# Kernel tuning notes

Measured on AMD Instinct MI355X. Metric: run time of the kernel, lower is better.

Reference implementation:

```python
import jax, jax.numpy as jnp
import numpy as np

N_NODES = 100000
N_EDGES = 1600000
N_GRAPHS = 2048
EPS = 1e-5


def gcn_conv(x, src, dst, W, b):
    # PyG GCNConv: add self-loops, symmetric normalization D^-1/2 (A+I) D^-1/2, then linear.
    xw = x @ W  # [N, F]
    deg = jax.ops.segment_sum(jnp.ones((src.shape[0],), xw.dtype), dst, num_segments=N_NODES) + 1.0
    dinv = jax.lax.rsqrt(deg)  # deg >= 1 due to self loops
    norm = dinv[src] * dinv[dst]  # [E]
    msg = xw[src] * norm[:, None]  # gather + scale
    agg = jax.ops.segment_sum(msg, dst, num_segments=N_NODES)
    agg = agg + xw * (dinv * dinv)[:, None]  # self-loop term
    return agg + b


def bn_eval(h, gamma, beta, rm, rv):
    return (h - rm) * jax.lax.rsqrt(rv + EPS) * gamma + beta


def setup_inputs() -> dict:
    key = jax.random.key(0)
    ks = jax.random.split(key, 12)
    x = jax.random.normal(ks[0], (N_NODES, 74), jnp.float32)
    edge_index = jax.random.randint(ks[1], (2, N_EDGES), 0, N_NODES, dtype=jnp.int64)
    batch = jnp.sort(jax.random.randint(ks[2], (N_NODES,), 0, N_GRAPHS, dtype=jnp.int64))
    def lin(k, fi, fo):
        return jax.random.normal(k, (fi, fo), jnp.float32) / np.sqrt(fi)
    return {
        "x": x, "edge_index": edge_index, "batch": batch,
        "W1": lin(ks[3], 74, 256), "b1": jnp.zeros((256,), jnp.float32),
        "g1": jnp.ones((256,), jnp.float32), "beta1": jnp.zeros((256,), jnp.float32),
        "rm1": jax.random.normal(ks[4], (256,), jnp.float32) * 0.1,
        "rv1": jax.random.uniform(ks[5], (256,), jnp.float32, 0.5, 1.5),
        "W2": lin(ks[6], 256, 256), "b2": jnp.zeros((256,), jnp.float32),
        "g2": jnp.ones((256,), jnp.float32), "beta2": jnp.zeros((256,), jnp.float32),
        "rm2": jax.random.normal(ks[7], (256,), jnp.float32) * 0.1,
        "rv2": jax.random.uniform(ks[8], (256,), jnp.float32, 0.5, 1.5),
        "W3": lin(ks[9], 256, 384), "b3": jnp.zeros((384,), jnp.float32),
    }


def reference(x, edge_index, batch, W1, b1, g1, beta1, rm1, rv1,
              W2, b2, g2, beta2, rm2, rv2, W3, b3):
    src, dst = edge_index[0], edge_index[1]
    h1 = jax.nn.relu(bn_eval(gcn_conv(x, src, dst, W1, b1), g1, beta1, rm1, rv1))
    h2 = jax.nn.relu(bn_eval(gcn_conv(h1, src, dst, W2, b2), g2, beta2, rm2, rv2))
    h3 = gcn_conv(h2, src, dst, W3, b3)
    # global_mean_pool + global_max_pool over batch segments
    cnt = jax.ops.segment_sum(jnp.ones((N_NODES,), h3.dtype), batch, num_segments=N_GRAPHS)
    mean_pool = jax.ops.segment_sum(h3, batch, num_segments=N_GRAPHS) / jnp.maximum(cnt, 1.0)[:, None]
    max_pool = jax.ops.segment_max(h3, batch, num_segments=N_GRAPHS)
    return mean_pool + max_pool
```

## Files before the change

### kernel.cpp

```cpp
#include <hip/hip_runtime.h>

typedef __bf16 bf16x8 __attribute__((ext_vector_type(8)));
typedef float f32x4 __attribute__((ext_vector_type(4)));
typedef float f32x2 __attribute__((ext_vector_type(2)));
typedef unsigned short ushort4v __attribute__((ext_vector_type(4)));
typedef unsigned short ushort8v __attribute__((ext_vector_type(8)));

__device__ __forceinline__ unsigned short f2b(float f) {
  unsigned u = __float_as_uint(f);
  unsigned r = u + 0x7FFFu + ((u >> 16) & 1u);
  return (unsigned short)(r >> 16);
}
__device__ __forceinline__ float b2f(unsigned short v) {
  return __uint_as_float(((unsigned)v) << 16);
}

__device__ __forceinline__ void fp8x4_to_f32(unsigned w, float out[4]) {
#if __has_builtin(__builtin_amdgcn_cvt_pk_f32_fp8)
  f32x2 lo = __builtin_amdgcn_cvt_pk_f32_fp8(w, false);
  f32x2 hi = __builtin_amdgcn_cvt_pk_f32_fp8(w, true);
  out[0] = lo[0]; out[1] = lo[1]; out[2] = hi[0]; out[3] = hi[1];
#else
#pragma unroll
  for (int i = 0; i < 4; ++i) {
    unsigned u = (w >> (8 * i)) & 0xffu;
    unsigned em = u & 0x7fu;
    float nrm = __uint_as_float((em + 960u) << 20);
    float sub = (float)em * 0x1p-9f;
    float mag = (em >= 8u) ? nrm : sub;
    out[i] = (u & 0x80u) ? -mag : mag;
  }
#endif
}

__device__ __forceinline__ unsigned char f32_to_fp8(float f) {
  float a = fabsf(f);
  unsigned s = (__float_as_uint(f) >> 31) << 7;
  a = fminf(a, 448.0f);
  unsigned r;
  if (a >= 0x1p-6f) {
    unsigned b = __float_as_uint(a);
    unsigned m = b & 0x7fffffu;
    int ei = (int)(b >> 23) - 127;
    unsigned mr = (m + 0x80000u) >> 20;
    unsigned ee = (unsigned)(ei + 7) + (mr >> 3);
    mr &= 7u;
    if (ee >= 16u) { ee = 15u; mr = 6u; }
    r = (ee << 3) | mr;
  } else {
    unsigned m = (unsigned)(a * 512.0f + 0.5f);
    r = m;
  }
  return (unsigned char)(s | r);
}

static constexpr int SCAN_CHUNK = 1024;

__global__ void k_bnprep(const float* __restrict__ g, const float* __restrict__ beta,
                         const float* __restrict__ rm, const float* __restrict__ rv,
                         const float* __restrict__ b, int n,
                         float* __restrict__ scale, float* __restrict__ shift) {
  int i = blockIdx.x * blockDim.x + threadIdx.x;
  if (i < n) {
    float s = g[i] * rsqrtf(rv[i] + 1e-5f);
    scale[i] = s;
    shift[i] = (b[i] - rm[i]) * s + beta[i];
  }
}

__global__ void k_edge_count(const int* __restrict__ dst, int E, int* __restrict__ cnt) {
  int i = blockIdx.x * blockDim.x + threadIdx.x;
  if (i < E) atomicAdd(&cnt[dst[i]], 1);
}

__global__ void k_dinv(const int* __restrict__ cnt, int n, float* __restrict__ dinv) {
  int i = blockIdx.x * blockDim.x + threadIdx.x;
  if (i < n) dinv[i] = rsqrtf(1.0f + (float)cnt[i]);
}

__global__ void k_wt(const float* __restrict__ W, int K, int N, int Kp,
                     unsigned short* __restrict__ Wt) {
  int idx = blockIdx.x * blockDim.x + threadIdx.x;
  if (idx >= N * Kp) return;
  int n = idx / Kp, k = idx - n * Kp;
  Wt[idx] = f2b(k < K ? W[(size_t)k * N + n] : 0.0f);
}

__global__ void k_x2b(const float* __restrict__ x, const float* __restrict__ dinv, int n,
                      unsigned short* __restrict__ xb) {
  int idx = blockIdx.x * blockDim.x + threadIdx.x;
  if (idx >= n * 20) return;
  int row = idx / 20, j = idx - row * 20;
  int f0 = j * 4;
  float dv = dinv[row];
  ushort4v o;
#pragma unroll
  for (int j2 = 0; j2 < 4; ++j2) {
    int f = f0 + j2;
    o[j2] = (f < 74) ? f2b(dv * x[(size_t)row * 74 + f]) : (unsigned short)0;
  }
  *(ushort4v*)(xb + (size_t)row * 80 + f0) = o;
}

__global__ void k_gbounds(const int* __restrict__ batch, int n, int* __restrict__ gstart,
                          int* __restrict__ gend) {
  int i = blockIdx.x * blockDim.x + threadIdx.x;
  if (i >= n) return;
  int g = batch[i];
  if (i == 0 || batch[i - 1] != g) gstart[g] = i;
  if (i == n - 1 || batch[i + 1] != g) gend[g] = i + 1;
}

__global__ void k_chunk_sum(const int* __restrict__ cnt, int n, int* __restrict__ bsum) {
  __shared__ int s[256];
  int base = blockIdx.x * SCAN_CHUNK;
  int t = threadIdx.x;
  int v = 0;
  for (int i = t; i < SCAN_CHUNK; i += 256) {
    int idx = base + i;
    v += (idx < n) ? cnt[idx] : 0;
  }
  s[t] = v;
  __syncthreads();
  for (int o = 128; o > 0; o >>= 1) {
    if (t < o) s[t] += s[t + o];
    __syncthreads();
  }
  if (t == 0) bsum[blockIdx.x] = s[0];
}

__global__ void k_scan_bsum(int* __restrict__ bsum, int nb) {
  if (threadIdx.x == 0 && blockIdx.x == 0) {
    int acc = 0;
    for (int i = 0; i < nb; ++i) { int v = bsum[i]; bsum[i] = acc; acc += v; }
  }
}

__global__ void k_write_rowptr(const int* __restrict__ cnt, int n, const int* __restrict__ bsum,
                               int* __restrict__ rowptr, int E) {
  __shared__ int s[256];
  __shared__ int sx[257];
  int base = blockIdx.x * SCAN_CHUNK;
  int t = threadIdx.x;
  int loc[4];
  int sum = 0;
#pragma unroll
  for (int j = 0; j < 4; ++j) {
    int idx = base + t * 4 + j;
    int c = (idx < n) ? cnt[idx] : 0;
    loc[j] = sum;
    sum += c;
  }
  s[t] = sum;
  __syncthreads();
  if (t == 0) {
    int acc = 0;
    for (int i = 0; i < 256; ++i) { sx[i] = acc; acc += s[i]; }
  }
  __syncthreads();
  int off = bsum[blockIdx.x] + sx[t];
#pragma unroll
  for (int j = 0; j < 4; ++j) {
    int idx = base + t * 4 + j;
    if (idx < n) rowptr[idx] = off + loc[j];
  }
  if (blockIdx.x == 0 && t == 0) rowptr[n] = E;
}

__global__ void k_fill(const int* __restrict__ src, const int* __restrict__ dst, int E,
                       const int* __restrict__ rowptr, int* __restrict__ cursor,
                       int* __restrict__ colA) {
  int e = blockIdx.x * blockDim.x + threadIdx.x;
  if (e < E) {
    int d = dst[e];
    int p = atomicAdd(&cursor[d], 1);
    colA[rowptr[d] + p] = src[e];
  }
}

__global__ __launch_bounds__(256) void k_aggregate74b(const unsigned short* __restrict__ xb,
                                                      const int* __restrict__ rowptr,
                                                      const int* __restrict__ colA,
                                                      const float* __restrict__ dinv, int n,
                                                      unsigned short* __restrict__ out) {
  int wid = (int)((blockIdx.x * (size_t)blockDim.x + threadIdx.x) >> 6);
  int lane = threadIdx.x & 63;
  if (wid >= n) return;
  int half = lane >> 5, hl = lane & 31;
  bool act = hl < 20;
  float acc[4] = {0.0f, 0.0f, 0.0f, 0.0f};
  int e0 = rowptr[wid], e1 = rowptr[wid + 1];
  int e = e0;
  for (; e + 7 < e1; e += 8) {
    int b = e + half * 4;
    int s0 = colA[b], s1 = colA[b + 1], s2 = colA[b + 2], s3 = colA[b + 3];
    ushort4v v0 = {}, v1 = {}, v2 = {}, v3 = {};
    if (act) {
      v0 = *(const ushort4v*)(xb + (size_t)s0 * 80 + hl * 4);
      v1 = *(const ushort4v*)(xb + (size_t)s1 * 80 + hl * 4);
      v2 = *(const ushort4v*)(xb + (size_t)s2 * 80 + hl * 4);
      v3 = *(const ushort4v*)(xb + (size_t)s3 * 80 + hl * 4);
    }
#pragma unroll
    for (int j = 0; j < 4; ++j)
      acc[j] += (b2f(v0[j]) + b2f(v1[j])) + (b2f(v2[j]) + b2f(v3[j]));
  }
  for (int t = e + half; t < e1; t += 2) {
    int s = colA[t];
    ushort4v v = {};
    if (act) v = *(const ushort4v*)(xb + (size_t)s * 80 + hl * 4);
#pragma unroll
    for (int j = 0; j < 4; ++j) acc[j] += b2f(v[j]);
  }
#pragma unroll
  for (int j = 0; j < 4; ++j) acc[j] += __shfl_xor(acc[j], 32);
  if (half == 0) {
    float di = dinv[wid];
    if (act) {
      ushort4v sv = *(const ushort4v*)(xb + (size_t)wid * 80 + hl * 4);
      ushort4v o;
#pragma unroll
      for (int j = 0; j < 4; ++j) o[j] = f2b(di * (acc[j] + b2f(sv[j])));
      *(ushort4v*)(out + (size_t)wid * 128 + hl * 4) = o;
    } else {
      ushort4v z = {};
      *(ushort4v*)(out + (size_t)wid * 128 + 80 + (hl - 20) * 4) = z;
    }
  }
}

__global__ __launch_bounds__(256) void k_aggregate256(const unsigned char* __restrict__ h8,
                                                      const int* __restrict__ rowptr,
                                                      const int* __restrict__ colA,
                                                      const float* __restrict__ dinv, int n,
                                                      unsigned short* __restrict__ out) {
  int wid = (int)((blockIdx.x * (size_t)blockDim.x + threadIdx.x) >> 6);
  int lane = threadIdx.x & 63;
  if (wid >= n) return;
  float acc[4];
  {
    unsigned w = *(const unsigned*)(h8 + (size_t)wid * 256 + lane * 4);
    fp8x4_to_f32(w, acc);
  }
  int e0 = rowptr[wid], e1 = rowptr[wid + 1];
  int e = e0;
  for (; e + 7 < e1; e += 8) {
    int c[8];
    unsigned w[8];
#pragma unroll
    for (int q = 0; q < 8; ++q) c[q] = colA[e + q];
#pragma unroll
    for (int q = 0; q < 8; ++q)
      w[q] = *(const unsigned*)(h8 + (size_t)c[q] * 256 + lane * 4);
#pragma unroll
    for (int q = 0; q < 8; ++q) {
      float v[4];
      fp8x4_to_f32(w[q], v);
#pragma unroll
      for (int j = 0; j < 4; ++j) acc[j] += v[j];
    }
  }
  for (; e < e1; ++e) {
    unsigned w = *(const unsigned*)(h8 + (size_t)colA[e] * 256 + lane * 4);
    float v[4];
    fp8x4_to_f32(w, v);
#pragma unroll
    for (int j = 0; j < 4; ++j) acc[j] += v[j];
  }
  float di = dinv[wid];
  ushort4v o;
#pragma unroll
  for (int j = 0; j < 4; ++j) o[j] = f2b(di * acc[j]);
  *(ushort4v*)(out + (size_t)wid * 256 + lane * 4) = o;
}

template <int EPI>
__global__ __launch_bounds__(256) void k_gemm_mfma(const unsigned short* __restrict__ A,
                                                   const unsigned short* __restrict__ Bt,
                                                   int M, int N, int K,
                                                   const float* __restrict__ scale,
                                                   const float* __restrict__ shift,
                                                   const float* __restrict__ dinv,
                                                   unsigned char* __restrict__ C8,
                                                   unsigned short* __restrict__ C16) {
  __shared__ __align__(16) unsigned short Ast[128 * 64];
  __shared__ __align__(16) unsigned short Bst[64 * 64];
  const int t = threadIdx.x;
  const int lane = t & 63;
  const int wid = t >> 6;
  const int wm = wid >> 1, wn = wid & 1;
  const int lr = lane >> 4, lc = lane & 15;
  const int m0 = blockIdx.y * 128;
  const int n0 = blockIdx.x * 64;
  f32x4 acc[4][2] = {};
  char* astB = (char*)Ast;
  char* bstB = (char*)Bst;

  for (int kb = 0; kb < K; kb += 64) {
#pragma unroll
    for (int i = 0; i < 4; ++i) {
      int c = t + 256 * i;
      int row = c >> 3, slot = c & 7;
      int gm = m0 + row;
      ushort8v v = {};
      if (gm < M) v = *(const ushort8v*)(A + (size_t)gm * K + kb + slot * 8);
      int byte = row * 128 + slot * 16;
      *(ushort8v*)(astB + (byte ^ ((row & 7) << 4))) = v;
    }
#pragma unroll
    for (int i = 0; i < 2; ++i) {
      int c = t + 256 * i;
      int row = c >> 3, slot = c & 7;
      ushort8v v = *(const ushort8v*)(Bt + (size_t)(n0 + row) * K + kb + slot * 8);
      int byte = row * 128 + slot * 16;
      *(ushort8v*)(bstB + (byte ^ ((row & 7) << 4))) = v;
    }
    __syncthreads();
#pragma unroll
    for (int kk = 0; kk < 2; ++kk) {
      bf16x8 a[4], b[2];
      int kbyte = lr * 16 + kk * 64;
#pragma unroll
      for (int mi = 0; mi < 4; ++mi) {
        int row = wm * 64 + mi * 16 + lc;
        int byte = row * 128 + kbyte;
        a[mi] = *(const bf16x8*)(astB + (byte ^ ((row & 7) << 4)));
      }
#pragma unroll
      for (int ni = 0; ni < 2; ++ni) {
        int row = wn * 32 + ni * 16 + lc;
        int byte = row * 128 + kbyte;
        b[ni] = *(const bf16x8*)(bstB + (byte ^ ((row & 7) << 4)));
      }
#pragma unroll
      for (int mi = 0; mi < 4; ++mi)
#pragma unroll
        for (int ni = 0; ni < 2; ++ni)
          acc[mi][ni] =
              __builtin_amdgcn_mfma_f32_16x16x32_bf16(a[mi], b[ni], acc[mi][ni], 0, 0, 0);
    }
    __syncthreads();
  }

#pragma unroll
  for (int ni = 0; ni < 2; ++ni) {
    int colx = n0 + wn * 32 + ni * 16 + lc;
    float sc = (EPI == 0) ? scale[colx] : 0.0f;
    float sh = shift[colx];
#pragma unroll
    for (int mi = 0; mi < 4; ++mi) {
      int rbase = m0 + wm * 64 + mi * 16 + lr * 4;
#pragma unroll
      for (int r = 0; r < 4; ++r) {
        int row = rbase + r;
        if (row < M) {
          float v = acc[mi][ni][r];
          if (EPI == 0) {
            v = fmaxf(fmaf(v, sc, sh), 0.0f) * dinv[row];
            C8[(size_t)row * N + colx] = f32_to_fp8(v);
          } else {
            v += sh;
            C16[(size_t)row * N + colx] = f2b(v);
          }
        }
      }
    }
  }
}

__global__ __launch_bounds__(384) void k_pool(const unsigned short* __restrict__ h3,
                                              const int* __restrict__ gstart,
                                              const int* __restrict__ gend, int NF,
                                              float* __restrict__ out) {
  int g = blockIdx.x;
  int t = threadIdx.x;
  int s = gstart[g], e = gend[g];
  if (s >= 0 && e > s) {
    float sum = 0.0f, mx = -3.4e38f;
    for (int r = s; r < e; ++r) {
      float v = b2f(h3[(size_t)r * NF + t]);
      sum += v;
      mx = fmaxf(mx, v);
    }
    out[(size_t)g * NF + t] = sum / (float)(e - s) + mx;
  } else {
    out[(size_t)g * NF + t] = -INFINITY;
  }
}

extern "C" void kernel_launch(void* const* d_in, const int* in_sizes, int n_in, void* d_out,
                              int out_size, void* d_ws, size_t ws_size, hipStream_t stream) {
  const float* x    = (const float*)d_in[0];
  const int* edge   = (const int*)d_in[1];
  const int* batch  = (const int*)d_in[2];
  const float* W1   = (const float*)d_in[3];
  const float* b1   = (const float*)d_in[4];
  const float* g1   = (const float*)d_in[5];
  const float* be1  = (const float*)d_in[6];
  const float* rm1  = (const float*)d_in[7];
  const float* rv1  = (const float*)d_in[8];
  const float* W2   = (const float*)d_in[9];
  const float* b2   = (const float*)d_in[10];
  const float* g2   = (const float*)d_in[11];
  const float* be2  = (const float*)d_in[12];
  const float* rm2  = (const float*)d_in[13];
  const float* rv2  = (const float*)d_in[14];
  const float* W3   = (const float*)d_in[15];
  const float* b3   = (const float*)d_in[16];

  const int NN = in_sizes[2];
  const int E  = in_sizes[1] / 2;
  const int F1 = in_sizes[4];
  const int F3 = in_sizes[16];
  const int NG = out_size / F3;
  const int K1p = 128;
  const int* srcv = edge;
  const int* dstv = edge + E;

  char* p = (char*)d_ws;
  auto carve = [&](size_t bytes) -> char* {
    char* r = p;
    p += (bytes + 255) & ~(size_t)255;
    return r;
  };
  float* dinv           = (float*)carve((size_t)NN * 4);
  int* cnt              = (int*)carve((size_t)NN * 4);
  int* rowptr           = (int*)carve((size_t)(NN + 1) * 4);
  int* cursor           = (int*)carve((size_t)NN * 4);
  int* bsum             = (int*)carve(4096);
  int* colA             = (int*)carve((size_t)E * 4);
  float* scale1         = (float*)carve((size_t)F1 * 4);
  float* shift1         = (float*)carve((size_t)F1 * 4);
  float* scale2         = (float*)carve((size_t)F1 * 4);
  float* shift2         = (float*)carve((size_t)F1 * 4);
  unsigned short* W1t   = (unsigned short*)carve((size_t)F1 * K1p * 2);
  unsigned short* W2t   = (unsigned short*)carve((size_t)F1 * F1 * 2);
  unsigned short* W3t   = (unsigned short*)carve((size_t)F3 * F1 * 2);
  int* gstart           = (int*)carve((size_t)NG * 4);
  int* gend             = (int*)carve((size_t)NG * 4);
  unsigned short* xb    = (unsigned short*)carve((size_t)NN * 80 * 2);
  unsigned char* h8     = (unsigned char*)carve((size_t)NN * F1);
  unsigned short* agg   = (unsigned short*)carve((size_t)NN * F1 * 2);
  unsigned short* h3    = (unsigned short*)carve((size_t)NN * F3 * 2);
  (void)ws_size; (void)n_in;

  hipMemsetAsync(cnt, 0, (size_t)NN * 4, stream);
  hipMemsetAsync(cursor, 0, (size_t)NN * 4, stream);
  hipMemsetAsync(gstart, 0xFF, (size_t)NG * 4, stream);
  hipMemsetAsync(gend, 0, (size_t)NG * 4, stream);
  k_bnprep<<<1, 256, 0, stream>>>(g1, be1, rm1, rv1, b1, F1, scale1, shift1);
  k_bnprep<<<1, 256, 0, stream>>>(g2, be2, rm2, rv2, b2, F1, scale2, shift2);
  k_wt<<<(F1 * K1p + 255) / 256, 256, 0, stream>>>(W1, 74, F1, K1p, W1t);
  k_wt<<<(F1 * F1 + 255) / 256, 256, 0, stream>>>(W2, F1, F1, F1, W2t);
  k_wt<<<(F3 * F1 + 255) / 256, 256, 0, stream>>>(W3, F1, F3, F1, W3t);
  k_gbounds<<<(NN + 255) / 256, 256, 0, stream>>>(batch, NN, gstart, gend);

  k_edge_count<<<(E + 255) / 256, 256, 0, stream>>>(dstv, E, cnt);
  k_dinv<<<(NN + 255) / 256, 256, 0, stream>>>(cnt, NN, dinv);
  k_x2b<<<(NN * 20 + 255) / 256, 256, 0, stream>>>(x, dinv, NN, xb);

  int nchunks = (NN + SCAN_CHUNK - 1) / SCAN_CHUNK;
  k_chunk_sum<<<nchunks, 256, 0, stream>>>(cnt, NN, bsum);
  k_scan_bsum<<<1, 64, 0, stream>>>(bsum, nchunks);
  k_write_rowptr<<<nchunks, 256, 0, stream>>>(cnt, NN, bsum, rowptr, E);
  k_fill<<<(E + 255) / 256, 256, 0, stream>>>(srcv, dstv, E, rowptr, cursor, colA);

  dim3 blk(256);
  int aggBlocks = (NN + 3) / 4;
  int gy = (NN + 127) / 128;

  k_aggregate74b<<<aggBlocks, blk, 0, stream>>>(xb, rowptr, colA, dinv, NN, agg);
  {
    dim3 grid(F1 / 64, gy);
    k_gemm_mfma<0><<<grid, blk, 0, stream>>>(agg, W1t, NN, F1, K1p, scale1, shift1, dinv,
                                             h8, nullptr);
  }
  k_aggregate256<<<aggBlocks, blk, 0, stream>>>(h8, rowptr, colA, dinv, NN, agg);
  {
    dim3 grid(F1 / 64, gy);
    k_gemm_mfma<0><<<grid, blk, 0, stream>>>(agg, W2t, NN, F1, F1, scale2, shift2, dinv,
                                             h8, nullptr);
  }
  k_aggregate256<<<aggBlocks, blk, 0, stream>>>(h8, rowptr, colA, dinv, NN, agg);
  {
    dim3 grid(F3 / 64, gy);
    k_gemm_mfma<1><<<grid, blk, 0, stream>>>(agg, W3t, NN, F3, F1, nullptr, b3, dinv,
                                             nullptr, h3);
  }
  k_pool<<<NG, 384, 0, stream>>>(h3, gstart, gend, F3, (float*)d_out);
}
```

Before: 744.5 us.

## Build CSR via two-level bucketing by destination with shared-memory local scan

Replaces the global count/scan/fill CSR construction with a bucket pass that packs (src, local dst) per 128-node bucket, a single-block scan of bucket sizes, and a per-bucket kernel that counts, scans and scatters edges in shared memory while also computing dinv. This cuts global atomics on per-node counters and several kernel launches. It risks silently dropping edges if a bucket exceeds its fixed capacity. It also caps the scan at 1024 buckets and source ids at 17 bits, and reuses the h3 buffer as scratch.

```diff
diff --git a/kernel.cpp b/kernel.cpp
--- a/kernel.cpp
+++ b/kernel.cpp
@@ -54,7 +54,8 @@
   return (unsigned char)(s | r);
 }
 
-static constexpr int SCAN_CHUNK = 1024;
+static constexpr int BUCKET_NODES = 128;
+static constexpr int BUCKET_CAP = 4096;
 
 __global__ void k_bnprep(const float* __restrict__ g, const float* __restrict__ beta,
                          const float* __restrict__ rm, const float* __restrict__ rv,
@@ -68,16 +69,6 @@
   }
 }
 
-__global__ void k_edge_count(const int* __restrict__ dst, int E, int* __restrict__ cnt) {
-  int i = blockIdx.x * blockDim.x + threadIdx.x;
-  if (i < E) atomicAdd(&cnt[dst[i]], 1);
-}
-
-__global__ void k_dinv(const int* __restrict__ cnt, int n, float* __restrict__ dinv) {
-  int i = blockIdx.x * blockDim.x + threadIdx.x;
-  if (i < n) dinv[i] = rsqrtf(1.0f + (float)cnt[i]);
-}
-
 __global__ void k_wt(const float* __restrict__ W, int K, int N, int Kp,
                      unsigned short* __restrict__ Wt) {
   int idx = blockIdx.x * blockDim.x + threadIdx.x;
@@ -111,70 +102,79 @@
   if (i == n - 1 || batch[i + 1] != g) gend[g] = i + 1;
 }
 
-__global__ void k_chunk_sum(const int* __restrict__ cnt, int n, int* __restrict__ bsum) {
-  __shared__ int s[256];
-  int base = blockIdx.x * SCAN_CHUNK;
+__global__ void k_bucket(const int* __restrict__ src, const int* __restrict__ dst, int E,
+                         int* __restrict__ bcur, unsigned* __restrict__ bdata) {
+  int i = blockIdx.x * blockDim.x + threadIdx.x;
+  if (i < E) {
+    int d = dst[i];
+    int b = d >> 7;
+    int dl = d & 127;
+    int pos = atomicAdd(&bcur[b], 1);
+    if (pos < BUCKET_CAP)
+      bdata[(size_t)b * BUCKET_CAP + pos] = (unsigned)src[i] | ((unsigned)dl << 17);
+  }
+}
+
+__global__ void k_scanb(const int* __restrict__ bcur, int NB, int* __restrict__ bbase,
+                        int* __restrict__ rowptr, int NN) {
+  __shared__ int s[1024];
   int t = threadIdx.x;
-  int v = 0;
-  for (int i = t; i < SCAN_CHUNK; i += 256) {
-    int idx = base + i;
-    v += (idx < n) ? cnt[idx] : 0;
-  }
+  int v = (t < NB) ? min(bcur[t], BUCKET_CAP) : 0;
   s[t] = v;
   __syncthreads();
-  for (int o = 128; o > 0; o >>= 1) {
-    if (t < o) s[t] += s[t + o];
-    __syncthreads();
-  }
-  if (t == 0) bsum[blockIdx.x] = s[0];
-}
-
-__global__ void k_scan_bsum(int* __restrict__ bsum, int nb) {
-  if (threadIdx.x == 0 && blockIdx.x == 0) {
-    int acc = 0;
-    for (int i = 0; i < nb; ++i) { int v = bsum[i]; bsum[i] = acc; acc += v; }
-  }
-}
-
-__global__ void k_write_rowptr(const int* __restrict__ cnt, int n, const int* __restrict__ bsum,
-                               int* __restrict__ rowptr, int E) {
-  __shared__ int s[256];
-  __shared__ int sx[257];
-  int base = blockIdx.x * SCAN_CHUNK;
+  for (int o = 1; o < 1024; o <<= 1) {
+    int x = (t >= o) ? s[t - o] : 0;
+    __syncthreads();
+    s[t] += x;
+    __syncthreads();
+  }
+  if (t < NB) bbase[t] = s[t] - v;
+  if (t == 0) rowptr[NN] = s[1023];
+}
+
+__global__ __launch_bounds__(256) void k_bucket_csr(const unsigned* __restrict__ bdata,
+                                                    const int* __restrict__ bcur,
+                                                    const int* __restrict__ bbase, int NN,
+                                                    int* __restrict__ rowptr,
+                                                    float* __restrict__ dinv,
+                                                    int* __restrict__ colA) {
+  __shared__ int lcnt[BUCKET_NODES];
+  __shared__ int lpre[BUCKET_NODES];
+  __shared__ int lcur[BUCKET_NODES];
+  int b = blockIdx.x;
   int t = threadIdx.x;
-  int loc[4];
-  int sum = 0;
-#pragma unroll
-  for (int j = 0; j < 4; ++j) {
-    int idx = base + t * 4 + j;
-    int c = (idx < n) ? cnt[idx] : 0;
-    loc[j] = sum;
-    sum += c;
-  }
-  s[t] = sum;
+  int n0 = b * BUCKET_NODES;
+  int ne = min(bcur[b], BUCKET_CAP);
+  const unsigned* bd = bdata + (size_t)b * BUCKET_CAP;
+  if (t < BUCKET_NODES) lcnt[t] = 0;
   __syncthreads();
-  if (t == 0) {
-    int acc = 0;
-    for (int i = 0; i < 256; ++i) { sx[i] = acc; acc += s[i]; }
-  }
+  for (int i = t; i < ne; i += 256) atomicAdd(&lcnt[bd[i] >> 17], 1);
   __syncthreads();
-  int off = bsum[blockIdx.x] + sx[t];
-#pragma unroll
-  for (int j = 0; j < 4; ++j) {
-    int idx = base + t * 4 + j;
-    if (idx < n) rowptr[idx] = off + loc[j];
-  }
-  if (blockIdx.x == 0 && t == 0) rowptr[n] = E;
-}
-
-__global__ void k_fill(const int* __restrict__ src, const int* __restrict__ dst, int E,
-                       const int* __restrict__ rowptr, int* __restrict__ cursor,
-                       int* __restrict__ colA) {
-  int e = blockIdx.x * blockDim.x + threadIdx.x;
-  if (e < E) {
-    int d = dst[e];
-    int p = atomicAdd(&cursor[d], 1);
-    colA[rowptr[d] + p] = src[e];
+  if (t < BUCKET_NODES) lpre[t] = lcnt[t];
+  __syncthreads();
+#pragma unroll
+  for (int o = 1; o < BUCKET_NODES; o <<= 1) {
+    int x = (t < BUCKET_NODES && t >= o) ? lpre[t - o] : 0;
+    __syncthreads();
+    if (t < BUCKET_NODES) lpre[t] += x;
+    __syncthreads();
+  }
+  int base = bbase[b];
+  if (t < BUCKET_NODES) {
+    lpre[t] -= lcnt[t];
+    int node = n0 + t;
+    if (node < NN) {
+      rowptr[node] = base + lpre[t];
+      dinv[node] = rsqrtf(1.0f + (float)lcnt[t]);
+    }
+    lcur[t] = 0;
+  }
+  __syncthreads();
+  for (int i = t; i < ne; i += 256) {
+    unsigned pk = bd[i];
+    int dl = pk >> 17;
+    int slot = base + lpre[dl] + atomicAdd(&lcur[dl], 1);
+    colA[slot] = (int)(pk & 0x1FFFFu);
   }
 }
 
@@ -414,6 +414,7 @@
   const int F3 = in_sizes[16];
   const int NG = out_size / F3;
   const int K1p = 128;
+  const int NB = (NN + BUCKET_NODES - 1) / BUCKET_NODES;
   const int* srcv = edge;
   const int* dstv = edge + E;
 
@@ -424,10 +425,9 @@
     return r;
   };
   float* dinv           = (float*)carve((size_t)NN * 4);
-  int* cnt              = (int*)carve((size_t)NN * 4);
   int* rowptr           = (int*)carve((size_t)(NN + 1) * 4);
-  int* cursor           = (int*)carve((size_t)NN * 4);
-  int* bsum             = (int*)carve(4096);
+  int* bcur             = (int*)carve((size_t)NB * 4);
+  int* bbase            = (int*)carve((size_t)NB * 4);
   int* colA             = (int*)carve((size_t)E * 4);
   float* scale1         = (float*)carve((size_t)F1 * 4);
   float* shift1         = (float*)carve((size_t)F1 * 4);
@@ -442,10 +442,10 @@
   unsigned char* h8     = (unsigned char*)carve((size_t)NN * F1);
   unsigned short* agg   = (unsigned short*)carve((size_t)NN * F1 * 2);
   unsigned short* h3    = (unsigned short*)carve((size_t)NN * F3 * 2);
+  unsigned* bdata       = (unsigned*)h3;
   (void)ws_size; (void)n_in;
 
-  hipMemsetAsync(cnt, 0, (size_t)NN * 4, stream);
-  hipMemsetAsync(cursor, 0, (size_t)NN * 4, stream);
+  hipMemsetAsync(bcur, 0, (size_t)NB * 4, stream);
   hipMemsetAsync(gstart, 0xFF, (size_t)NG * 4, stream);
   hipMemsetAsync(gend, 0, (size_t)NG * 4, stream);
   k_bnprep<<<1, 256, 0, stream>>>(g1, be1, rm1, rv1, b1, F1, scale1, shift1);
@@ -455,15 +455,11 @@
   k_wt<<<(F3 * F1 + 255) / 256, 256, 0, stream>>>(W3, F1, F3, F1, W3t);
   k_gbounds<<<(NN + 255) / 256, 256, 0, stream>>>(batch, NN, gstart, gend);
 
-  k_edge_count<<<(E + 255) / 256, 256, 0, stream>>>(dstv, E, cnt);
-  k_dinv<<<(NN + 255) / 256, 256, 0, stream>>>(cnt, NN, dinv);
+  k_bucket<<<(E + 255) / 256, 256, 0, stream>>>(srcv, dstv, E, bcur, bdata);
+  k_scanb<<<1, 1024, 0, stream>>>(bcur, NB, bbase, rowptr, NN);
+  k_bucket_csr<<<NB, 256, 0, stream>>>(bdata, bcur, bbase, NN, rowptr, dinv, colA);
+
   k_x2b<<<(NN * 20 + 255) / 256, 256, 0, stream>>>(x, dinv, NN, xb);
-
-  int nchunks = (NN + SCAN_CHUNK - 1) / SCAN_CHUNK;
-  k_chunk_sum<<<nchunks, 256, 0, stream>>>(cnt, NN, bsum);
-  k_scan_bsum<<<1, 64, 0, stream>>>(bsum, nchunks);
-  k_write_rowptr<<<nchunks, 256, 0, stream>>>(cnt, NN, bsum, rowptr, E);
-  k_fill<<<(E + 255) / 256, 256, 0, stream>>>(srcv, dstv, E, rowptr, cursor, colA);
 
   dim3 blk(256);
   int aggBlocks = (NN + 3) / 4;
```

Measured after the change: 948.7 us. 1.27x slower.
